# Kernel optimization log

Hardware: AMD Instinct MI355X
Metric: run time of the kernel (lower is better)

The kernel has to match this reference:

```python
import jax, jax.numpy as jnp
import numpy as np

N = 50000      # nodes
E = 800000     # edges (before self-loops)
IN = 64        # in_dim
C = 64         # hidden_dim (per-head out channels)
H = 4          # heads
NEG_SLOPE = 0.2


def setup_inputs() -> dict:
    key = jax.random.key(0)
    ks = jax.random.split(key, 9)
    x = jax.random.normal(ks[0], (N, IN), jnp.float32)
    edge_index = jax.random.randint(ks[1], (2, E), 0, N)
    edge_attr = jax.random.uniform(ks[2], (E, 1), jnp.float32)
    s_in = 1.0 / np.sqrt(IN)
    s_c = 1.0 / np.sqrt(C)
    W = jax.random.normal(ks[3], (IN, H * C), jnp.float32) * s_in
    att_src = jax.random.normal(ks[4], (H, C), jnp.float32) * s_c
    att_dst = jax.random.normal(ks[5], (H, C), jnp.float32) * s_c
    lin_edge_w = jax.random.normal(ks[6], (1, H * C), jnp.float32)
    att_edge = jax.random.normal(ks[7], (H, C), jnp.float32) * s_c
    bias = jnp.zeros((C,), jnp.float32)
    return dict(x=x, edge_index=edge_index, edge_attr=edge_attr, W=W,
                att_src=att_src, att_dst=att_dst, lin_edge_w=lin_edge_w,
                att_edge=att_edge, bias=bias)


def reference(x, edge_index, edge_attr, W, att_src, att_dst, lin_edge_w, att_edge, bias):
    n = x.shape[0]
    # add self-loops (PyG default add_self_loops=True, fill_value='mean')
    loop = jnp.arange(n)
    src = jnp.concatenate([edge_index[0], loop])          # [E+N]
    dst = jnp.concatenate([edge_index[1], loop])          # [E+N]
    ea = jnp.concatenate([edge_attr,
                          jnp.full((n, 1), edge_attr.mean(), edge_attr.dtype)], axis=0)
    # node transform: [N, H, C]
    h = (x @ W).reshape(n, H, C)
    a_src = jnp.einsum('nhc,hc->nh', h, att_src)          # [N, H]
    a_dst = jnp.einsum('nhc,hc->nh', h, att_dst)          # [N, H]
    eh = (ea @ lin_edge_w).reshape(-1, H, C)              # [E+N, H, C]
    a_edge = jnp.einsum('ehc,hc->eh', eh, att_edge)       # [E+N, H]
    # per-edge attention logit
    alpha = a_src[src] + a_dst[dst] + a_edge              # [E+N, H]
    alpha = jax.nn.leaky_relu(alpha, NEG_SLOPE)
    # segment softmax over edges grouped by destination node
    amax = jax.ops.segment_max(alpha, dst, num_segments=n)
    alpha = jnp.exp(alpha - amax[dst])
    asum = jax.ops.segment_sum(alpha, dst, num_segments=n)
    alpha = alpha / (asum[dst] + 1e-16)                   # [E+N, H]
    # weighted message + scatter-add aggregation
    msg = h[src] * alpha[..., None]                       # [E+N, H, C]
    out = jax.ops.segment_sum(msg, dst, num_segments=n)   # [N, H, C]
    out = out.mean(axis=1) + bias                         # concat=False -> head mean
    # ReLU + residual
    return jax.nn.relu(out) + x
```

## Files before the change

kernel.cpp:

```cpp
#include <hip/hip_runtime.h>
#include <hip/hip_fp16.h>
#include <math.h>

#define H 4
#define C 64
#define HC 256
#define NEG 0.2f
#define MAXDEG 64
#define XPAD 72
#define HPAD 264

typedef __attribute__((ext_vector_type(8))) _Float16 half8;
typedef __attribute__((ext_vector_type(4))) float f32x4;
typedef float f32x2 __attribute__((vector_size(8)));

__global__ __launch_bounds__(256) void phase1_kernel(
    const float* __restrict__ x, const float* __restrict__ W,
    const float* __restrict__ att_src, const float* __restrict__ att_dst,
    const int* __restrict__ ei, const float* __restrict__ edge_attr,
    unsigned char* __restrict__ h, float* __restrict__ a_src, float* __restrict__ a_dst,
    unsigned* __restrict__ counts, unsigned* __restrict__ edges,
    float* __restrict__ mean_acc, int Nn, int Ee, int G1, int G2) {
    int t = threadIdx.x;
    if ((int)blockIdx.x < G1) {
        __shared__ __align__(16) _Float16 xs[16 * XPAD];
        __shared__ __align__(16) _Float16 hs[16 * HPAD];
        int w = t >> 6, lane = t & 63, quad = lane >> 4, c16 = lane & 15;
        half8 bf[4][2];
#pragma unroll
        for (int nt = 0; nt < 4; ++nt)
#pragma unroll
            for (int kh = 0; kh < 2; ++kh)
#pragma unroll
                for (int j = 0; j < 8; ++j)
                    bf[nt][kh][j] = (_Float16)W[(kh * 32 + quad * 8 + j) * HC +
                                                w * 64 + nt * 16 + c16];
        float ats[4], atd[4];
#pragma unroll
        for (int nt = 0; nt < 4; ++nt) {
            ats[nt] = att_src[w * 64 + nt * 16 + c16];
            atd[nt] = att_dst[w * 64 + nt * 16 + c16];
        }

        int nTiles = (Nn + 15) >> 4;
        for (int mt = blockIdx.x; mt < nTiles; mt += G1) {
            __syncthreads();
            {
                int row = t >> 4, col4 = (t & 15) * 4;
                int node = mt * 16 + row;
                float4 v = make_float4(0.f, 0.f, 0.f, 0.f);
                if (node < Nn) v = *(const float4*)(x + (size_t)node * 64 + col4);
                _Float16* dst = xs + row * XPAD + col4;
                dst[0] = (_Float16)v.x; dst[1] = (_Float16)v.y;
                dst[2] = (_Float16)v.z; dst[3] = (_Float16)v.w;
            }
            __syncthreads();
            half8 a0 = *(const half8*)(xs + c16 * XPAD + quad * 8);
            half8 a1 = *(const half8*)(xs + c16 * XPAD + 32 + quad * 8);
            f32x4 d[4];
#pragma unroll
            for (int nt = 0; nt < 4; ++nt) {
                f32x4 acc = {0.f, 0.f, 0.f, 0.f};
                acc = __builtin_amdgcn_mfma_f32_16x16x32_f16(a0, bf[nt][0], acc, 0, 0, 0);
                acc = __builtin_amdgcn_mfma_f32_16x16x32_f16(a1, bf[nt][1], acc, 0, 0, 0);
                d[nt] = acc;
            }
#pragma unroll
            for (int reg = 0; reg < 4; ++reg) {
                float ps = 0.f, pd = 0.f;
#pragma unroll
                for (int nt = 0; nt < 4; ++nt) {
                    ps += d[nt][reg] * ats[nt];
                    pd += d[nt][reg] * atd[nt];
                }
                ps += __shfl_xor(ps, 1); pd += __shfl_xor(pd, 1);
                ps += __shfl_xor(ps, 2); pd += __shfl_xor(pd, 2);
                ps += __shfl_xor(ps, 4); pd += __shfl_xor(pd, 4);
                ps += __shfl_xor(ps, 8); pd += __shfl_xor(pd, 8);
                if (c16 == 0) {
                    int node = mt * 16 + quad * 4 + reg;
                    if (node < Nn) {
                        a_src[node * 4 + w] = ps;
                        a_dst[node * 4 + w] = pd;
                    }
                }
            }
#pragma unroll
            for (int nt = 0; nt < 4; ++nt)
#pragma unroll
                for (int reg = 0; reg < 4; ++reg)
                    hs[(quad * 4 + reg) * HPAD + w * 64 + nt * 16 + c16] =
                        (_Float16)d[nt][reg];
            __syncthreads();
            {
                int row = t >> 4, chunk = t & 15;
                int node = mt * 16 + row;
                if (node < Nn) {
                    const uint4* sp = (const uint4*)(hs + row * HPAD + chunk * 16);
                    uint4 sA = sp[0], sB = sp[1];
                    unsigned ua[8] = {sA.x, sA.y, sA.z, sA.w, sB.x, sB.y, sB.z, sB.w};
                    unsigned ow[4];
#pragma unroll
                    for (int q = 0; q < 4; ++q) {
                        float2 p0 = __half22float2(*reinterpret_cast<const __half2*>(&ua[q * 2]));
                        float2 p1 = __half22float2(*reinterpret_cast<const __half2*>(&ua[q * 2 + 1]));
                        int v = __builtin_amdgcn_cvt_pk_fp8_f32(p0.x, p0.y, 0, false);
                        v = __builtin_amdgcn_cvt_pk_fp8_f32(p1.x, p1.y, v, true);
                        ow[q] = (unsigned)v;
                    }
                    *(uint4*)(h + (size_t)node * HC + chunk * 16) =
                        make_uint4(ow[0], ow[1], ow[2], ow[3]);
                }
            }
        }
    } else {
        __shared__ float red[256];
        int gid = ((int)blockIdx.x - G1) * 256 + t;
        int stride = G2 * 256;
        float s = 0.f;
        for (int i = gid; i < Ee; i += stride) {
            int src = ei[i];
            int dst = ei[Ee + i];
            float ea = edge_attr[i];
            s += ea;
            unsigned q = (unsigned)(ea * 65535.f + 0.5f);
            unsigned rank = atomicAdd(&counts[dst], 1u);
            if (rank < MAXDEG)
                edges[(size_t)dst * MAXDEG + rank] = (q << 16) | (unsigned)src;
        }
        red[t] = s;
        __syncthreads();
        for (int o = 128; o; o >>= 1) {
            if (t < o) red[t] += red[t + o];
            __syncthreads();
        }
        if (t == 0) atomicAdd(mean_acc, red[0]);
    }
}

__global__ __launch_bounds__(256) void aggregate_kernel(
    const unsigned* __restrict__ counts, const unsigned* __restrict__ edges,
    const float* __restrict__ a_src, const float* __restrict__ a_dst,
    const float* __restrict__ lin_edge_w, const float* __restrict__ att_edge,
    const float* __restrict__ mean_acc, const unsigned char* __restrict__ h,
    const float* __restrict__ bias, const float* __restrict__ x,
    float* __restrict__ out, int Nn, float invE) {
    int lane = threadIdx.x & 63;
    int n = blockIdx.x * 4 + (threadIdx.x >> 6);
    if (n >= Nn) return;
    int head = lane >> 4;

    int sub = lane & 15;
    float kp = 0.f;
#pragma unroll
    for (int j = 0; j < 4; ++j) {
        int c = sub * 4 + j;
        kp += lin_edge_w[head * C + c] * att_edge[head * C + c];
    }
    kp += __shfl_xor(kp, 1);
    kp += __shfl_xor(kp, 2);
    kp += __shfl_xor(kp, 4);
    kp += __shfl_xor(kp, 8);
    float K = kp;
    const float DEQ = 1.0f / 65535.f;

    float mean = mean_acc[0] * invE;
    unsigned deg = counts[n];
    if (deg > MAXDEG) deg = MAXDEG;
    size_t base = (size_t)n * MAXDEG;
    float ad = a_dst[n * 4 + head];
    const unsigned* h8 = (const unsigned*)h;

    float ls = a_src[n * 4 + head] + ad + mean * K;
    ls = ls > 0.f ? ls : NEG * ls;
    float wsl = __expf(ls);
    unsigned sv = h8[(size_t)n * 64 + lane];
    f32x2 s01 = __builtin_amdgcn_cvt_pk_f32_fp8((int)sv, false);
    f32x2 s23 = __builtin_amdgcn_cvt_pk_f32_fp8((int)sv, true);
    float4 acc = make_float4(wsl * s01[0], wsl * s01[1], wsl * s23[0], wsl * s23[1]);
    float swgt = wsl;

    int i = 0;
    for (; i + 4 <= (int)deg; i += 4) {
        unsigned r0 = edges[base + i + 0];
        unsigned r1 = edges[base + i + 1];
        unsigned r2 = edges[base + i + 2];
        unsigned r3 = edges[base + i + 3];
        int s0 = r0 & 0xFFFF, s1 = r1 & 0xFFFF, s2 = r2 & 0xFFFF, s3 = r3 & 0xFFFF;
        unsigned hv0 = h8[(size_t)s0 * 64 + lane];
        unsigned hv1 = h8[(size_t)s1 * 64 + lane];
        unsigned hv2 = h8[(size_t)s2 * 64 + lane];
        unsigned hv3 = h8[(size_t)s3 * 64 + lane];
        float l0 = a_src[s0 * 4 + head] + ad + (float)(r0 >> 16) * DEQ * K;
        float l1 = a_src[s1 * 4 + head] + ad + (float)(r1 >> 16) * DEQ * K;
        float l2 = a_src[s2 * 4 + head] + ad + (float)(r2 >> 16) * DEQ * K;
        float l3 = a_src[s3 * 4 + head] + ad + (float)(r3 >> 16) * DEQ * K;
        l0 = l0 > 0.f ? l0 : NEG * l0;
        l1 = l1 > 0.f ? l1 : NEG * l1;
        l2 = l2 > 0.f ? l2 : NEG * l2;
        l3 = l3 > 0.f ? l3 : NEG * l3;
        float w0 = __expf(l0), w1 = __expf(l1), w2 = __expf(l2), w3 = __expf(l3);
        swgt += (w0 + w1) + (w2 + w3);
        {
            f32x2 f01 = __builtin_amdgcn_cvt_pk_f32_fp8((int)hv0, false);
            f32x2 f23 = __builtin_amdgcn_cvt_pk_f32_fp8((int)hv0, true);
            acc.x += w0 * f01[0]; acc.y += w0 * f01[1];
            acc.z += w0 * f23[0]; acc.w += w0 * f23[1];
        }
        {
            f32x2 f01 = __builtin_amdgcn_cvt_pk_f32_fp8((int)hv1, false);
            f32x2 f23 = __builtin_amdgcn_cvt_pk_f32_fp8((int)hv1, true);
            acc.x += w1 * f01[0]; acc.y += w1 * f01[1];
            acc.z += w1 * f23[0]; acc.w += w1 * f23[1];
        }
        {
            f32x2 f01 = __builtin_amdgcn_cvt_pk_f32_fp8((int)hv2, false);
            f32x2 f23 = __builtin_amdgcn_cvt_pk_f32_fp8((int)hv2, true);
            acc.x += w2 * f01[0]; acc.y += w2 * f01[1];
            acc.z += w2 * f23[0]; acc.w += w2 * f23[1];
        }
        {
            f32x2 f01 = __builtin_amdgcn_cvt_pk_f32_fp8((int)hv3, false);
            f32x2 f23 = __builtin_amdgcn_cvt_pk_f32_fp8((int)hv3, true);
            acc.x += w3 * f01[0]; acc.y += w3 * f01[1];
            acc.z += w3 * f23[0]; acc.w += w3 * f23[1];
        }
    }
    for (; i < (int)deg; ++i) {
        unsigned r = edges[base + i];
        int s0 = r & 0xFFFF;
        unsigned hv = h8[(size_t)s0 * 64 + lane];
        float l = a_src[s0 * 4 + head] + ad + (float)(r >> 16) * DEQ * K;
        l = l > 0.f ? l : NEG * l;
        float wg = __expf(l);
        swgt += wg;
        f32x2 f01 = __builtin_amdgcn_cvt_pk_f32_fp8((int)hv, false);
        f32x2 f23 = __builtin_amdgcn_cvt_pk_f32_fp8((int)hv, true);
        acc.x += wg * f01[0]; acc.y += wg * f01[1];
        acc.z += wg * f23[0]; acc.w += wg * f23[1];
    }

    float inv = 1.f / (swgt + 1e-16f);
    acc.x *= inv; acc.y *= inv; acc.z *= inv; acc.w *= inv;

    acc.x += __shfl_xor(acc.x, 16);
    acc.y += __shfl_xor(acc.y, 16);
    acc.z += __shfl_xor(acc.z, 16);
    acc.w += __shfl_xor(acc.w, 16);
    acc.x += __shfl_xor(acc.x, 32);
    acc.y += __shfl_xor(acc.y, 32);
    acc.z += __shfl_xor(acc.z, 32);
    acc.w += __shfl_xor(acc.w, 32);
    if (lane < 16) {
        float4 b = ((const float4*)bias)[lane];
        float4 xv = ((const float4*)x)[(size_t)n * 16 + lane];
        float4 o;
        o.x = fmaxf(acc.x * 0.25f + b.x, 0.f) + xv.x;
        o.y = fmaxf(acc.y * 0.25f + b.y, 0.f) + xv.y;
        o.z = fmaxf(acc.z * 0.25f + b.z, 0.f) + xv.z;
        o.w = fmaxf(acc.w * 0.25f + b.w, 0.f) + xv.w;
        ((float4*)out)[(size_t)n * 16 + lane] = o;
    }
}

extern "C" void kernel_launch(void* const* d_in, const int* in_sizes, int n_in,
                              void* d_out, int out_size, void* d_ws, size_t ws_size,
                              hipStream_t stream) {
    const float* x = (const float*)d_in[0];
    const int* ei = (const int*)d_in[1];
    const float* edge_attr = (const float*)d_in[2];
    const float* W = (const float*)d_in[3];
    const float* att_src = (const float*)d_in[4];
    const float* att_dst = (const float*)d_in[5];
    const float* lin_edge_w = (const float*)d_in[6];
    const float* att_edge = (const float*)d_in[7];
    const float* bias = (const float*)d_in[8];
    float* out = (float*)d_out;
    int Nn = in_sizes[0] / 64;
    int Ee = in_sizes[1] / 2;

    char* p = (char*)d_ws;
    size_t off = 0;
    auto alloc = [&](size_t bytes) -> char* {
        char* r = p + off;
        off += (bytes + 255) & ~(size_t)255;
        return r;
    };
    float* mean_acc = (float*)alloc(256);
    unsigned* counts = (unsigned*)alloc((size_t)Nn * 4);
    size_t zero_bytes = off;
    unsigned* edges = (unsigned*)alloc((size_t)Nn * MAXDEG * 4);
    unsigned char* h = (unsigned char*)alloc((size_t)Nn * HC);
    float* a_src = (float*)alloc((size_t)Nn * H * 4);
    float* a_dst = (float*)alloc((size_t)Nn * H * 4);
    (void)ws_size;

    const int G1 = 512, G2 = 1536;
    hipMemsetAsync(d_ws, 0, zero_bytes, stream);
    phase1_kernel<<<G1 + G2, 256, 0, stream>>>(x, W, att_src, att_dst, ei, edge_attr,
                                               h, a_src, a_dst, counts, edges,
                                               mean_acc, Nn, Ee, G1, G2);
    aggregate_kernel<<<(Nn + 3) / 4, 256, 0, stream>>>(counts, edges, a_src, a_dst,
                                                       lin_edge_w, att_edge, mean_acc,
                                                       h, bias, x, out, Nn,
                                                       1.0f / (float)Ee);
}
```

Baseline: 174.7 us.

## Partition edge bucketing and aggregation by destination range per XCD

```diff
diff --git a/kernel.cpp b/kernel.cpp
--- a/kernel.cpp
+++ b/kernel.cpp
@@ -9,6 +9,7 @@
 #define MAXDEG 64
 #define XPAD 72
 #define HPAD 264
+#define NXCD 8
 
 typedef __attribute__((ext_vector_type(8))) _Float16 half8;
 typedef __attribute__((ext_vector_type(4))) float f32x4;
@@ -20,7 +21,7 @@
     const int* __restrict__ ei, const float* __restrict__ edge_attr,
     unsigned char* __restrict__ h, float* __restrict__ a_src, float* __restrict__ a_dst,
     unsigned* __restrict__ counts, unsigned* __restrict__ edges,
-    float* __restrict__ mean_acc, int Nn, int Ee, int G1, int G2) {
+    float* __restrict__ mean_acc, int Nn, int Ee, int G1, int G2, int npb) {
     int t = threadIdx.x;
     if ((int)blockIdx.x < G1) {
         __shared__ __align__(16) _Float16 xs[16 * XPAD];
@@ -115,18 +116,24 @@
         }
     } else {
         __shared__ float red[256];
-        int gid = ((int)blockIdx.x - G1) * 256 + t;
-        int stride = G2 * 256;
+        int sb = (int)blockIdx.x - G1;
+        int g = sb & (NXCD - 1);
+        int bi = sb >> 3;
+        int nGrpBlk = G2 >> 3;
+        int lo = g * npb;
+        int hi = min(lo + npb, Nn);
         float s = 0.f;
-        for (int i = gid; i < Ee; i += stride) {
+        for (int i = bi * 256 + t; i < Ee; i += nGrpBlk * 256) {
+            int dst = ei[Ee + i];
             int src = ei[i];
-            int dst = ei[Ee + i];
             float ea = edge_attr[i];
-            s += ea;
-            unsigned q = (unsigned)(ea * 65535.f + 0.5f);
-            unsigned rank = atomicAdd(&counts[dst], 1u);
-            if (rank < MAXDEG)
-                edges[(size_t)dst * MAXDEG + rank] = (q << 16) | (unsigned)src;
+            if (dst >= lo && dst < hi) {
+                s += ea;
+                unsigned q = (unsigned)(ea * 65535.f + 0.5f);
+                unsigned rank = atomicAdd(&counts[dst], 1u);
+                if (rank < MAXDEG)
+                    edges[(size_t)dst * MAXDEG + rank] = (q << 16) | (unsigned)src;
+            }
         }
         red[t] = s;
         __syncthreads();
@@ -144,17 +151,19 @@
     const float* __restrict__ lin_edge_w, const float* __restrict__ att_edge,
     const float* __restrict__ mean_acc, const unsigned char* __restrict__ h,
     const float* __restrict__ bias, const float* __restrict__ x,
-    float* __restrict__ out, int Nn, float invE) {
+    float* __restrict__ out, int Nn, float invE, int npb) {
     int lane = threadIdx.x & 63;
-    int n = blockIdx.x * 4 + (threadIdx.x >> 6);
-    if (n >= Nn) return;
+    int g = blockIdx.x & (NXCD - 1);
+    int j = blockIdx.x >> 3;
+    int n = g * npb + j * 4 + (threadIdx.x >> 6);
+    if (n >= min((g + 1) * npb, Nn)) return;
     int head = lane >> 4;
 
     int sub = lane & 15;
     float kp = 0.f;
 #pragma unroll
-    for (int j = 0; j < 4; ++j) {
-        int c = sub * 4 + j;
+    for (int jj = 0; jj < 4; ++jj) {
+        int c = sub * 4 + jj;
         kp += lin_edge_w[head * C + c] * att_edge[head * C + c];
     }
     kp += __shfl_xor(kp, 1);
@@ -278,6 +287,7 @@
     float* out = (float*)d_out;
     int Nn = in_sizes[0] / 64;
     int Ee = in_sizes[1] / 2;
+    int npb = (Nn + NXCD - 1) / NXCD;
 
     char* p = (char*)d_ws;
     size_t off = 0;
@@ -296,12 +306,13 @@
     (void)ws_size;
 
     const int G1 = 512, G2 = 1536;
+    int aggBlocks = NXCD * ((npb + 3) / 4);
     hipMemsetAsync(d_ws, 0, zero_bytes, stream);
     phase1_kernel<<<G1 + G2, 256, 0, stream>>>(x, W, att_src, att_dst, ei, edge_attr,
                                                h, a_src, a_dst, counts, edges,
-                                               mean_acc, Nn, Ee, G1, G2);
-    aggregate_kernel<<<(Nn + 3) / 4, 256, 0, stream>>>(counts, edges, a_src, a_dst,
-                                                       lin_edge_w, att_edge, mean_acc,
-                                                       h, bias, x, out, Nn,
-                                                       1.0f / (float)Ee);
+                                               mean_acc, Nn, Ee, G1, G2, npb);
+    aggregate_kernel<<<aggBlocks, 256, 0, stream>>>(counts, edges, a_src, a_dst,
+                                                    lin_edge_w, att_edge, mean_acc,
+                                                    h, bias, x, out, Nn,
+                                                    1.0f / (float)Ee, npb);
 }
```

Result: no change. 177.6 us (+1.6%).
